# Kernel tuning notes

Hardware: AMD Instinct MI355X
Metric: run time of the kernel (lower is better)

Reference implementation:

```python
import jax, jax.numpy as jnp
import numpy as np

H = 16  # n_heads


def setup_inputs() -> dict:
    key = jax.random.key(0)
    ks = jax.random.split(key, 12)
    B, S, D = 16, 512, 1024
    inp = {
        "query": jax.random.normal(ks[0], (B, S, D), jnp.float32),
        "key": jax.random.normal(ks[1], (B, S, D), jnp.float32),
        "value": jax.random.normal(ks[2], (B, S, D), jnp.float32),
        "mask": jnp.ones((B, S), dtype=bool),
        "adj": jax.random.uniform(ks[3], (B, S, S), jnp.float32),
        # nn.Linear weights are [out, in]; y = x @ W.T + b
        "Wq": jax.random.normal(ks[4], (D, D), jnp.float32) / np.sqrt(D),
        "bq": jnp.zeros((D,), jnp.float32),
        "Wk": jax.random.normal(ks[5], (D, D), jnp.float32) / np.sqrt(D),
        "bk": jnp.zeros((D,), jnp.float32),
        "Wv": jax.random.normal(ks[6], (D, D), jnp.float32) / np.sqrt(D),
        "bv": jnp.zeros((D,), jnp.float32),
        "Wo": jax.random.normal(ks[7], (D, D), jnp.float32) / np.sqrt(D),
        "bo": jnp.zeros((D,), jnp.float32),
        "beta": jnp.array([0.5], jnp.float32),  # learned residual scale (init 0 in torch)
    }
    return inp


def reference(query, key, value, mask, adj, Wq, bq, Wk, bk, Wv, bv, Wo, bo, beta):
    B, S, D = query.shape
    h = H
    dk = D // h
    N = S * dk  # channel-attention "sequence" length

    def proj(x, W, b):
        # [B,S,D] -> [B,h,S,dk]
        return (x @ W.T + b).reshape(B, S, h, dk).transpose(0, 2, 1, 3)

    Q = proj(query, Wq, bq)
    K = proj(key, Wk, bk)
    V = proj(value, Wv, bv)

    # Flatten each head: [B, h, S*dk]; torch's q,k,v are the [B,N,h] transposes.
    Qf = Q.reshape(B, h, N)
    Kf = K.reshape(B, h, N)
    Vf = V.reshape(B, h, N)

    # channel attention: scores = q^T k / sqrt(h) -> [B,h,h]
    scores = jnp.einsum("bin,bjn->bij", Qf, Kf) / jnp.sqrt(jnp.asarray(h, Qf.dtype))
    attn = jax.nn.softmax(scores, axis=-1)  # dropout is identity at eval

    # x2 = attn @ v^T -> [B,h,N] -> view [B,h,S,dk]
    x2 = jnp.einsum("bij,bjn->bin", attn, Vf).reshape(B, h, S, dk)

    x = V + beta * x2                      # scaled residual on value
    x = x.transpose(0, 2, 1, 3).reshape(B, S, D)
    out = x @ Wo.T + bo
    return out, attn
```

## Files before the change

kernel.cpp:

```cpp
#include <hip/hip_runtime.h>
#include <cstdint>
#include <cstddef>


#define DIM 1024

typedef _Float16 f16_t;
typedef _Float16 f16x4_t __attribute__((ext_vector_type(4)));
typedef _Float16 f16x8_t __attribute__((ext_vector_type(8)));
typedef float    f32x4_t __attribute__((ext_vector_type(4)));

__device__ __forceinline__ void async_ld16(const void* g, void* l) {
    __builtin_amdgcn_global_load_lds((const __attribute__((address_space(1))) void*)g,
                                     (__attribute__((address_space(3))) void*)l,
                                     16, 0, 0);
}

__global__ __launch_bounds__(256) void pack_kernel(
    const float* __restrict__ q, const float* __restrict__ k, const float* __restrict__ v,
    const float* __restrict__ Wq, const float* __restrict__ Wk,
    const float* __restrict__ Wv, const float* __restrict__ Wo,
    f16_t* __restrict__ Aq, f16_t* __restrict__ Ak, f16_t* __restrict__ Av,
    f16_t* __restrict__ Bq, f16_t* __restrict__ Bk,
    f16_t* __restrict__ Bv, f16_t* __restrict__ Bo)
{
    const int u = blockIdx.x * 256 + threadIdx.x;
    const float* src; f16_t* dst; int i;
    if (u < 2097152)      { src = q;  dst = Aq; i = u; }
    else if (u < 4194304) { src = k;  dst = Ak; i = u - 2097152; }
    else if (u < 6291456) { src = v;  dst = Av; i = u - 4194304; }
    else if (u < 6553600) { src = Wq; dst = Bq; i = u - 6291456; }
    else if (u < 6815744) { src = Wk; dst = Bk; i = u - 6553600; }
    else if (u < 7077888) { src = Wv; dst = Bv; i = u - 6815744; }
    else                  { src = Wo; dst = Bo; i = u - 7077888; }
    float4 s = ((const float4*)src)[i];
    f16x4_t h;
    h[0] = (f16_t)s.x; h[1] = (f16_t)s.y; h[2] = (f16_t)s.z; h[3] = (f16_t)s.w;
    ((f16x4_t*)dst)[i] = h;
}

__device__ __forceinline__ void gemm_body(
    const f16_t* __restrict__ A, const f16_t* __restrict__ B,
    const float* __restrict__ bias, float* __restrict__ C, f16_t* __restrict__ C16,
    f16_t* As, f16_t* Bs, int tileM, int tileN)
{
    const int tid  = threadIdx.x;
    const int lane = tid & 63;
    const int w    = tid >> 6;
    const int wm = (w & 1) << 6;
    const int wn = (w >> 1) << 6;

    f32x4_t acc[4][4];
#pragma unroll
    for (int i = 0; i < 4; ++i)
#pragma unroll
        for (int j = 0; j < 4; ++j)
            acc[i][j] = (f32x4_t){0.f, 0.f, 0.f, 0.f};

    const int srow = lane >> 3;
    const int scol = ((lane & 7) ^ (lane >> 3)) << 3;
    const int arow = lane & 15;
    const int sx   = lane & 7;
    const int kqu  = lane >> 4;

    for (int kt = 0; kt < 16; ++kt) {
        const int k0 = kt << 6;
#pragma unroll
        for (int t = 0; t < 4; ++t) {
            const int row = (w << 5) + (t << 3);
            async_ld16(A + (size_t)(tileM + row + srow) * DIM + k0 + scol,
                       (void*)(As + row * 64));
            async_ld16(B + (size_t)(tileN + row + srow) * DIM + k0 + scol,
                       (void*)(Bs + row * 64));
        }
        __syncthreads();
#pragma unroll
        for (int kk = 0; kk < 2; ++kk) {
            const int cu = ((kk << 2) + kqu) ^ sx;
            f16x8_t af[4], bfv[4];
#pragma unroll
            for (int mt = 0; mt < 4; ++mt)
                af[mt] = *(const f16x8_t*)(As + (wm + (mt << 4) + arow) * 64 + (cu << 3));
#pragma unroll
            for (int nt = 0; nt < 4; ++nt)
                bfv[nt] = *(const f16x8_t*)(Bs + (wn + (nt << 4) + arow) * 64 + (cu << 3));
#pragma unroll
            for (int mt = 0; mt < 4; ++mt)
#pragma unroll
                for (int nt = 0; nt < 4; ++nt)
                    acc[mt][nt] = __builtin_amdgcn_mfma_f32_16x16x32_f16(
                        af[mt], bfv[nt], acc[mt][nt], 0, 0, 0);
        }
        __syncthreads();
    }

    const int rq = (lane >> 4) << 2;
    if (C16) {
#pragma unroll
        for (int nt = 0; nt < 4; ++nt) {
            const int col = tileN + wn + (nt << 4) + arow;
            const float bv = bias[col];
#pragma unroll
            for (int mt = 0; mt < 4; ++mt) {
                const int row = tileM + wm + (mt << 4) + rq;
#pragma unroll
                for (int r = 0; r < 4; ++r)
                    C16[(size_t)(row + r) * DIM + col] = (f16_t)(acc[mt][nt][r] + bv);
            }
        }
    } else {
#pragma unroll
        for (int nt = 0; nt < 4; ++nt) {
            const int col = tileN + wn + (nt << 4) + arow;
            const float bv = bias[col];
#pragma unroll
            for (int mt = 0; mt < 4; ++mt) {
                const int row = tileM + wm + (mt << 4) + rq;
#pragma unroll
                for (int r = 0; r < 4; ++r)
                    C[(size_t)(row + r) * DIM + col] = acc[mt][nt][r] + bv;
            }
        }
    }
}

struct Gemm3Args {
    const f16_t* A[3];
    const f16_t* B[3];
    const float* bias[3];
    f16_t*       C16[3];
};

__global__ __launch_bounds__(256) void gemm3(Gemm3Args args)
{
    __shared__ __align__(16) f16_t As[128 * 64];
    __shared__ __align__(16) f16_t Bs[128 * 64];
    const int z = blockIdx.z;
    gemm_body(args.A[z], args.B[z], args.bias[z], nullptr, args.C16[z],
              As, Bs, blockIdx.x * 128, blockIdx.y * 128);
}

__global__ __launch_bounds__(256) void gemm_o(
    const f16_t* __restrict__ A, const f16_t* __restrict__ B,
    const float* __restrict__ bias, float* __restrict__ C)
{
    __shared__ __align__(16) f16_t As[128 * 64];
    __shared__ __align__(16) f16_t Bs[128 * 64];
    gemm_body(A, B, bias, C, nullptr, As, Bs, blockIdx.x * 128, blockIdx.y * 128);
}

__global__ __launch_bounds__(256) void scores_kernel(
    const f16_t* __restrict__ Pq16, const f16_t* __restrict__ Pk16,
    float* __restrict__ part)
{
    __shared__ float red[4][256];
    const int b = blockIdx.x;
    const int slice = blockIdx.y;
    const int lane = threadIdx.x & 63;
    const int w = threadIdx.x >> 6;
    const int m  = lane & 15;
    const int q8 = (lane >> 4) << 3;

    f32x4_t acc = (f32x4_t){0.f, 0.f, 0.f, 0.f};
    const int s0 = slice * 32 + w * 8;
#pragma unroll
    for (int ss = 0; ss < 8; ++ss) {
        const size_t rb = (size_t)(b * 512 + s0 + ss) * DIM;
        const f16_t* qrow = Pq16 + rb;
        const f16_t* krow = Pk16 + rb;
#pragma unroll
        for (int c0 = 0; c0 < 64; c0 += 32) {
            f16x8_t af = *(const f16x8_t*)(qrow + m * 64 + c0 + q8);
            f16x8_t bf = *(const f16x8_t*)(krow + m * 64 + c0 + q8);
            acc = __builtin_amdgcn_mfma_f32_16x16x32_f16(af, bf, acc, 0, 0, 0);
        }
    }
    const int rq = (lane >> 4) << 2;
#pragma unroll
    for (int r = 0; r < 4; ++r)
        red[w][(rq + r) * 16 + m] = acc[r];
    __syncthreads();
    const int t = threadIdx.x;
    part[(size_t)(b * 16 + slice) * 256 + t] =
        red[0][t] + red[1][t] + red[2][t] + red[3][t];
}

__global__ __launch_bounds__(256) void softmax_kernel(
    const float* __restrict__ part, const float* __restrict__ beta_p,
    float* __restrict__ attn_out, float* __restrict__ Mm)
{
    const int t = threadIdx.x;
    const int b = t >> 4;
    const int i = t & 15;
    const float beta = beta_p[0];
    float s[16];
#pragma unroll
    for (int j = 0; j < 16; ++j) s[j] = 0.f;
#pragma unroll 4
    for (int sl = 0; sl < 16; ++sl) {
        const float* pp = part + (size_t)(b * 16 + sl) * 256 + i * 16;
#pragma unroll
        for (int j = 0; j < 16; ++j) s[j] += pp[j];
    }
    float mx = -1e30f;
#pragma unroll
    for (int j = 0; j < 16; ++j) {
        s[j] *= 0.25f;
        mx = fmaxf(mx, s[j]);
    }
    float sum = 0.f;
#pragma unroll
    for (int j = 0; j < 16; ++j) { s[j] = expf(s[j] - mx); sum += s[j]; }
    const float inv = 1.f / sum;
#pragma unroll
    for (int j = 0; j < 16; ++j) {
        float a = s[j] * inv;
        attn_out[t * 16 + j] = a;
        Mm[t * 16 + j] = beta * a + ((j == i) ? 1.f : 0.f);
    }
}

__global__ __launch_bounds__(256) void mix_kernel(
    const f16_t* __restrict__ Pv16, const float* __restrict__ Mm,
    f16_t* __restrict__ xmix)
{
    __shared__ float Msh[256];
    const int rbase = blockIdx.x * 8;
    const int b = rbase >> 9;
    Msh[threadIdx.x] = Mm[b * 256 + threadIdx.x];
    __syncthreads();
    const int w = threadIdx.x >> 6;
    const int lane = threadIdx.x & 63;
#pragma unroll
    for (int rr = 0; rr < 2; ++rr) {
        const int r = rbase + w * 2 + rr;
        const f16_t* vrow = Pv16 + (size_t)r * DIM;
        float v[16];
#pragma unroll
        for (int j = 0; j < 16; ++j) v[j] = (float)vrow[j * 64 + lane];
#pragma unroll
        for (int i = 0; i < 16; ++i) {
            float x = 0.f;
#pragma unroll
            for (int j = 0; j < 16; ++j) x += Msh[i * 16 + j] * v[j];
            xmix[(size_t)r * DIM + i * 64 + lane] = (f16_t)x;
        }
    }
}

extern "C" void kernel_launch(void* const* d_in, const int* in_sizes, int n_in,
                              void* d_out, int out_size, void* d_ws, size_t ws_size,
                              hipStream_t stream)
{
    (void)in_sizes; (void)n_in; (void)out_size; (void)ws_size;
    const float* q    = (const float*)d_in[0];
    const float* k    = (const float*)d_in[1];
    const float* v    = (const float*)d_in[2];
    const float* Wq   = (const float*)d_in[5];
    const float* bq   = (const float*)d_in[6];
    const float* Wk   = (const float*)d_in[7];
    const float* bk   = (const float*)d_in[8];
    const float* Wv   = (const float*)d_in[9];
    const float* bv   = (const float*)d_in[10];
    const float* Wo   = (const float*)d_in[11];
    const float* bo   = (const float*)d_in[12];
    const float* beta = (const float*)d_in[13];

    float* out  = (float*)d_out;
    float* attn = (float*)d_out + 8388608;

    char* p = (char*)d_ws;
    auto take = [&](size_t n) -> char* {
        char* cur = p; p += (n + 255) & ~(size_t)255; return cur;
    };
    f16_t* Aq = (f16_t*)take(16777216);
    f16_t* Ak = (f16_t*)take(16777216);
    f16_t* Av = (f16_t*)take(16777216);
    f16_t* Bq = (f16_t*)take(2097152);
    f16_t* Bk = (f16_t*)take(2097152);
    f16_t* Bv = (f16_t*)take(2097152);
    f16_t* Bo = (f16_t*)take(2097152);
    f16_t* Pq16 = (f16_t*)take(16777216);
    f16_t* Pk16 = (f16_t*)take(16777216);
    f16_t* Pv16 = (f16_t*)take(16777216);
    float* part = (float*)take(262144);
    float* Mm   = (float*)take(16384);
    f16_t* xmix = Aq;

    pack_kernel<<<28672, 256, 0, stream>>>(q, k, v, Wq, Wk, Wv, Wo,
                                           Aq, Ak, Av, Bq, Bk, Bv, Bo);

    Gemm3Args ga;
    ga.A[0] = Aq; ga.A[1] = Ak; ga.A[2] = Av;
    ga.B[0] = Bq; ga.B[1] = Bk; ga.B[2] = Bv;
    ga.bias[0] = bq; ga.bias[1] = bk; ga.bias[2] = bv;
    ga.C16[0] = Pq16; ga.C16[1] = Pk16; ga.C16[2] = Pv16;
    gemm3<<<dim3(64, 8, 3), 256, 0, stream>>>(ga);

    scores_kernel<<<dim3(16, 16), 256, 0, stream>>>(Pq16, Pk16, part);
    softmax_kernel<<<1, 256, 0, stream>>>(part, beta, attn, Mm);
    mix_kernel<<<1024, 256, 0, stream>>>(Pv16, Mm, xmix);
    gemm_o<<<dim3(64, 8), 256, 0, stream>>>(xmix, Bo, bo, out);
}
```

Baseline: 289.8 us.

## Fuse fp32-to-fp16 activation conversion into QKV GEMM and softmax into mix kernel

```diff
diff --git a/kernel.cpp b/kernel.cpp
--- a/kernel.cpp
+++ b/kernel.cpp
@@ -16,32 +16,27 @@
                                      16, 0, 0);
 }
 
-__global__ __launch_bounds__(256) void pack_kernel(
-    const float* __restrict__ q, const float* __restrict__ k, const float* __restrict__ v,
+__global__ __launch_bounds__(256) void pack_w(
     const float* __restrict__ Wq, const float* __restrict__ Wk,
     const float* __restrict__ Wv, const float* __restrict__ Wo,
-    f16_t* __restrict__ Aq, f16_t* __restrict__ Ak, f16_t* __restrict__ Av,
     f16_t* __restrict__ Bq, f16_t* __restrict__ Bk,
     f16_t* __restrict__ Bv, f16_t* __restrict__ Bo)
 {
     const int u = blockIdx.x * 256 + threadIdx.x;
     const float* src; f16_t* dst; int i;
-    if (u < 2097152)      { src = q;  dst = Aq; i = u; }
-    else if (u < 4194304) { src = k;  dst = Ak; i = u - 2097152; }
-    else if (u < 6291456) { src = v;  dst = Av; i = u - 4194304; }
-    else if (u < 6553600) { src = Wq; dst = Bq; i = u - 6291456; }
-    else if (u < 6815744) { src = Wk; dst = Bk; i = u - 6553600; }
-    else if (u < 7077888) { src = Wv; dst = Bv; i = u - 6815744; }
-    else                  { src = Wo; dst = Bo; i = u - 7077888; }
+    if (u < 262144)       { src = Wq; dst = Bq; i = u; }
+    else if (u < 524288)  { src = Wk; dst = Bk; i = u - 262144; }
+    else if (u < 786432)  { src = Wv; dst = Bv; i = u - 524288; }
+    else                  { src = Wo; dst = Bo; i = u - 786432; }
     float4 s = ((const float4*)src)[i];
     f16x4_t h;
     h[0] = (f16_t)s.x; h[1] = (f16_t)s.y; h[2] = (f16_t)s.z; h[3] = (f16_t)s.w;
     ((f16x4_t*)dst)[i] = h;
 }
 
-__device__ __forceinline__ void gemm_body(
-    const f16_t* __restrict__ A, const f16_t* __restrict__ B,
-    const float* __restrict__ bias, float* __restrict__ C, f16_t* __restrict__ C16,
+__device__ __forceinline__ void gemm_body_f32A(
+    const float* __restrict__ A, const f16_t* __restrict__ B,
+    const float* __restrict__ bias, f16_t* __restrict__ C16,
     f16_t* As, f16_t* Bs, int tileM, int tileN)
 {
     const int tid  = threadIdx.x;
@@ -63,11 +58,121 @@
     const int sx   = lane & 7;
     const int kqu  = lane >> 4;
 
+    int arows[4], acols[4];
+#pragma unroll
+    for (int s = 0; s < 4; ++s) {
+        const int n = tid + (s << 8);
+        arows[s] = n >> 3;
+        acols[s] = ((n & 7) ^ ((n >> 3) & 7)) << 3;
+    }
+
     for (int kt = 0; kt < 16; ++kt) {
         const int k0 = kt << 6;
 #pragma unroll
-        for (int t = 0; t < 4; ++t) {
-            const int row = (w << 5) + (t << 3);
+        for (int t4 = 0; t4 < 4; ++t4) {
+            const int row = (w << 5) + (t4 << 3);
+            async_ld16(B + (size_t)(tileN + row + srow) * DIM + k0 + scol,
+                       (void*)(Bs + row * 64));
+        }
+        float4 ld[4][2];
+#pragma unroll
+        for (int s = 0; s < 4; ++s) {
+            const float* src = A + (size_t)(tileM + arows[s]) * DIM + k0 + acols[s];
+            ld[s][0] = ((const float4*)src)[0];
+            ld[s][1] = ((const float4*)src)[1];
+        }
+#pragma unroll
+        for (int s = 0; s < 4; ++s) {
+            f16x8_t h;
+            h[0] = (f16_t)ld[s][0].x; h[1] = (f16_t)ld[s][0].y;
+            h[2] = (f16_t)ld[s][0].z; h[3] = (f16_t)ld[s][0].w;
+            h[4] = (f16_t)ld[s][1].x; h[5] = (f16_t)ld[s][1].y;
+            h[6] = (f16_t)ld[s][1].z; h[7] = (f16_t)ld[s][1].w;
+            *(f16x8_t*)(As + (tid + (s << 8)) * 8) = h;
+        }
+        __syncthreads();
+#pragma unroll
+        for (int kk = 0; kk < 2; ++kk) {
+            const int cu = ((kk << 2) + kqu) ^ sx;
+            f16x8_t af[4], bfv[4];
+#pragma unroll
+            for (int mt = 0; mt < 4; ++mt)
+                af[mt] = *(const f16x8_t*)(As + (wm + (mt << 4) + arow) * 64 + (cu << 3));
+#pragma unroll
+            for (int nt = 0; nt < 4; ++nt)
+                bfv[nt] = *(const f16x8_t*)(Bs + (wn + (nt << 4) + arow) * 64 + (cu << 3));
+#pragma unroll
+            for (int mt = 0; mt < 4; ++mt)
+#pragma unroll
+                for (int nt = 0; nt < 4; ++nt)
+                    acc[mt][nt] = __builtin_amdgcn_mfma_f32_16x16x32_f16(
+                        af[mt], bfv[nt], acc[mt][nt], 0, 0, 0);
+        }
+        __syncthreads();
+    }
+
+    const int rq = (lane >> 4) << 2;
+#pragma unroll
+    for (int nt = 0; nt < 4; ++nt) {
+        const int col = tileN + wn + (nt << 4) + arow;
+        const float bv = bias[col];
+#pragma unroll
+        for (int mt = 0; mt < 4; ++mt) {
+            const int row = tileM + wm + (mt << 4) + rq;
+#pragma unroll
+            for (int r = 0; r < 4; ++r)
+                C16[(size_t)(row + r) * DIM + col] = (f16_t)(acc[mt][nt][r] + bv);
+        }
+    }
+}
+
+struct Gemm3Args {
+    const float* A[3];
+    const f16_t* B[3];
+    const float* bias[3];
+    f16_t*       C16[3];
+};
+
+__global__ __launch_bounds__(256) void gemm3(Gemm3Args args)
+{
+    __shared__ __align__(16) f16_t As[128 * 64];
+    __shared__ __align__(16) f16_t Bs[128 * 64];
+    const int z = blockIdx.z;
+    gemm_body_f32A(args.A[z], args.B[z], args.bias[z], args.C16[z],
+                   As, Bs, blockIdx.x * 128, blockIdx.y * 128);
+}
+
+__global__ __launch_bounds__(256) void gemm_o(
+    const f16_t* __restrict__ A, const f16_t* __restrict__ B,
+    const float* __restrict__ bias, float* __restrict__ C)
+{
+    __shared__ __align__(16) f16_t As[128 * 64];
+    __shared__ __align__(16) f16_t Bs[128 * 64];
+    const int tileM = blockIdx.x * 128, tileN = blockIdx.y * 128;
+    const int tid  = threadIdx.x;
+    const int lane = tid & 63;
+    const int w    = tid >> 6;
+    const int wm = (w & 1) << 6;
+    const int wn = (w >> 1) << 6;
+
+    f32x4_t acc[4][4];
+#pragma unroll
+    for (int i = 0; i < 4; ++i)
+#pragma unroll
+        for (int j = 0; j < 4; ++j)
+            acc[i][j] = (f32x4_t){0.f, 0.f, 0.f, 0.f};
+
+    const int srow = lane >> 3;
+    const int scol = ((lane & 7) ^ (lane >> 3)) << 3;
+    const int arow = lane & 15;
+    const int sx   = lane & 7;
+    const int kqu  = lane >> 4;
+
+    for (int kt = 0; kt < 16; ++kt) {
+        const int k0 = kt << 6;
+#pragma unroll
+        for (int t4 = 0; t4 < 4; ++t4) {
+            const int row = (w << 5) + (t4 << 3);
             async_ld16(A + (size_t)(tileM + row + srow) * DIM + k0 + scol,
                        (void*)(As + row * 64));
             async_ld16(B + (size_t)(tileN + row + srow) * DIM + k0 + scol,
@@ -95,58 +200,18 @@
     }
 
     const int rq = (lane >> 4) << 2;
-    if (C16) {
-#pragma unroll
-        for (int nt = 0; nt < 4; ++nt) {
-            const int col = tileN + wn + (nt << 4) + arow;
-            const float bv = bias[col];
-#pragma unroll
-            for (int mt = 0; mt < 4; ++mt) {
-                const int row = tileM + wm + (mt << 4) + rq;
-#pragma unroll
-                for (int r = 0; r < 4; ++r)
-                    C16[(size_t)(row + r) * DIM + col] = (f16_t)(acc[mt][nt][r] + bv);
-            }
-        }
-    } else {
-#pragma unroll
-        for (int nt = 0; nt < 4; ++nt) {
-            const int col = tileN + wn + (nt << 4) + arow;
-            const float bv = bias[col];
-#pragma unroll
-            for (int mt = 0; mt < 4; ++mt) {
-                const int row = tileM + wm + (mt << 4) + rq;
-#pragma unroll
-                for (int r = 0; r < 4; ++r)
-                    C[(size_t)(row + r) * DIM + col] = acc[mt][nt][r] + bv;
-            }
-        }
-    }
-}
-
-struct Gemm3Args {
-    const f16_t* A[3];
-    const f16_t* B[3];
-    const float* bias[3];
-    f16_t*       C16[3];
-};
-
-__global__ __launch_bounds__(256) void gemm3(Gemm3Args args)
-{
-    __shared__ __align__(16) f16_t As[128 * 64];
-    __shared__ __align__(16) f16_t Bs[128 * 64];
-    const int z = blockIdx.z;
-    gemm_body(args.A[z], args.B[z], args.bias[z], nullptr, args.C16[z],
-              As, Bs, blockIdx.x * 128, blockIdx.y * 128);
-}
-
-__global__ __launch_bounds__(256) void gemm_o(
-    const f16_t* __restrict__ A, const f16_t* __restrict__ B,
-    const float* __restrict__ bias, float* __restrict__ C)
-{
-    __shared__ __align__(16) f16_t As[128 * 64];
-    __shared__ __align__(16) f16_t Bs[128 * 64];
-    gemm_body(A, B, bias, C, nullptr, As, Bs, blockIdx.x * 128, blockIdx.y * 128);
+#pragma unroll
+    for (int nt = 0; nt < 4; ++nt) {
+        const int col = tileN + wn + (nt << 4) + arow;
+        const float bv = bias[col];
+#pragma unroll
+        for (int mt = 0; mt < 4; ++mt) {
+            const int row = tileM + wm + (mt << 4) + rq;
+#pragma unroll
+            for (int r = 0; r < 4; ++r)
+                C[(size_t)(row + r) * DIM + col] = acc[mt][nt][r] + bv;
+        }
+    }
 }
 
 __global__ __launch_bounds__(256) void scores_kernel(
@@ -185,49 +250,49 @@
         red[0][t] + red[1][t] + red[2][t] + red[3][t];
 }
 
-__global__ __launch_bounds__(256) void softmax_kernel(
-    const float* __restrict__ part, const float* __restrict__ beta_p,
-    float* __restrict__ attn_out, float* __restrict__ Mm)
-{
-    const int t = threadIdx.x;
-    const int b = t >> 4;
-    const int i = t & 15;
-    const float beta = beta_p[0];
-    float s[16];
-#pragma unroll
-    for (int j = 0; j < 16; ++j) s[j] = 0.f;
-#pragma unroll 4
-    for (int sl = 0; sl < 16; ++sl) {
-        const float* pp = part + (size_t)(b * 16 + sl) * 256 + i * 16;
-#pragma unroll
-        for (int j = 0; j < 16; ++j) s[j] += pp[j];
-    }
-    float mx = -1e30f;
-#pragma unroll
-    for (int j = 0; j < 16; ++j) {
-        s[j] *= 0.25f;
-        mx = fmaxf(mx, s[j]);
-    }
-    float sum = 0.f;
-#pragma unroll
-    for (int j = 0; j < 16; ++j) { s[j] = expf(s[j] - mx); sum += s[j]; }
-    const float inv = 1.f / sum;
-#pragma unroll
-    for (int j = 0; j < 16; ++j) {
-        float a = s[j] * inv;
-        attn_out[t * 16 + j] = a;
-        Mm[t * 16 + j] = beta * a + ((j == i) ? 1.f : 0.f);
-    }
-}
-
 __global__ __launch_bounds__(256) void mix_kernel(
-    const f16_t* __restrict__ Pv16, const float* __restrict__ Mm,
-    f16_t* __restrict__ xmix)
+    const f16_t* __restrict__ Pv16, const float* __restrict__ part,
+    const float* __restrict__ beta_p,
+    float* __restrict__ attn_out, f16_t* __restrict__ xmix)
 {
     __shared__ float Msh[256];
     const int rbase = blockIdx.x * 8;
     const int b = rbase >> 9;
-    Msh[threadIdx.x] = Mm[b * 256 + threadIdx.x];
+    const int t = threadIdx.x;
+    if (t < 16) {
+        const int i = t;
+        float s[16];
+#pragma unroll
+        for (int j = 0; j < 16; ++j) s[j] = 0.f;
+#pragma unroll 4
+        for (int sl = 0; sl < 16; ++sl) {
+            const float* pp = part + (size_t)(b * 16 + sl) * 256 + i * 16;
+#pragma unroll
+            for (int j4 = 0; j4 < 4; ++j4) {
+                float4 v4 = ((const float4*)pp)[j4];
+                s[j4 * 4 + 0] += v4.x; s[j4 * 4 + 1] += v4.y;
+                s[j4 * 4 + 2] += v4.z; s[j4 * 4 + 3] += v4.w;
+            }
+        }
+        float mx = -1e30f;
+#pragma unroll
+        for (int j = 0; j < 16; ++j) {
+            s[j] *= 0.25f;
+            mx = fmaxf(mx, s[j]);
+        }
+        float sum = 0.f;
+#pragma unroll
+        for (int j = 0; j < 16; ++j) { s[j] = expf(s[j] - mx); sum += s[j]; }
+        const float inv = 1.f / sum;
+        const float beta = beta_p[0];
+        const bool wr_attn = (blockIdx.x & 63) == 0;
+#pragma unroll
+        for (int j = 0; j < 16; ++j) {
+            float a = s[j] * inv;
+            if (wr_attn) attn_out[(b * 16 + i) * 16 + j] = a;
+            Msh[i * 16 + j] = beta * a + ((j == i) ? 1.f : 0.f);
+        }
+    }
     __syncthreads();
     const int w = threadIdx.x >> 6;
     const int lane = threadIdx.x & 63;
@@ -273,9 +338,6 @@
     auto take = [&](size_t n) -> char* {
         char* cur = p; p += (n + 255) & ~(size_t)255; return cur;
     };
-    f16_t* Aq = (f16_t*)take(16777216);
-    f16_t* Ak = (f16_t*)take(16777216);
-    f16_t* Av = (f16_t*)take(16777216);
     f16_t* Bq = (f16_t*)take(2097152);
     f16_t* Bk = (f16_t*)take(2097152);
     f16_t* Bv = (f16_t*)take(2097152);
@@ -283,22 +345,19 @@
     f16_t* Pq16 = (f16_t*)take(16777216);
     f16_t* Pk16 = (f16_t*)take(16777216);
     f16_t* Pv16 = (f16_t*)take(16777216);
+    f16_t* xmix = (f16_t*)take(16777216);
     float* part = (float*)take(262144);
-    float* Mm   = (float*)take(16384);
-    f16_t* xmix = Aq;
-
-    pack_kernel<<<28672, 256, 0, stream>>>(q, k, v, Wq, Wk, Wv, Wo,
-                                           Aq, Ak, Av, Bq, Bk, Bv, Bo);
+
+    pack_w<<<4096, 256, 0, stream>>>(Wq, Wk, Wv, Wo, Bq, Bk, Bv, Bo);
 
     Gemm3Args ga;
-    ga.A[0] = Aq; ga.A[1] = Ak; ga.A[2] = Av;
+    ga.A[0] = q; ga.A[1] = k; ga.A[2] = v;
     ga.B[0] = Bq; ga.B[1] = Bk; ga.B[2] = Bv;
     ga.bias[0] = bq; ga.bias[1] = bk; ga.bias[2] = bv;
     ga.C16[0] = Pq16; ga.C16[1] = Pk16; ga.C16[2] = Pv16;
     gemm3<<<dim3(64, 8, 3), 256, 0, stream>>>(ga);
 
     scores_kernel<<<dim3(16, 16), 256, 0, stream>>>(Pq16, Pk16, part);
-    softmax_kernel<<<1, 256, 0, stream>>>(part, beta, attn, Mm);
-    mix_kernel<<<1024, 256, 0, stream>>>(Pv16, Mm, xmix);
+    mix_kernel<<<1024, 256, 0, stream>>>(Pv16, part, beta, attn, xmix);
     gemm_o<<<dim3(64, 8), 256, 0, stream>>>(xmix, Bo, bo, out);
 }
```

Measured after the change: 297.6 us. 2.7% more time.
